# Kernel tuning notes

Hardware: AMD Instinct MI355X
Metric: run time of the kernel (lower is better)

## Reference

```python
import jax, jax.numpy as jnp
import numpy as np


def _gcn_layer(x, W, b, src, dst, norm, n_nodes):
    # PyG GCNConv: h = x @ W, then degree-normalized scatter-add over edges (incl. self loops), then + bias
    h = x @ W                                   # [N, F_out]
    msg = h[src] * norm[:, None]                # [E+N, F_out]
    out = jax.ops.segment_sum(msg, dst, num_segments=n_nodes)
    return out + b


def _norm_and_loops(edge_index, n_nodes):
    # add self loops, compute symmetric normalization deg^-1/2[src]*deg^-1/2[dst]
    loop = jnp.arange(n_nodes, dtype=edge_index.dtype)
    src = jnp.concatenate([edge_index[0], loop])
    dst = jnp.concatenate([edge_index[1], loop])
    deg = jax.ops.segment_sum(jnp.ones_like(dst, dtype=jnp.float32), dst, num_segments=n_nodes)
    dinv = jnp.where(deg > 0, jax.lax.rsqrt(deg), 0.0)
    norm = dinv[src] * dinv[dst]
    return src, dst, norm


def setup_inputs() -> dict:
    key = jax.random.key(0)
    k1, k2, k3, k4 = jax.random.split(key, 4)
    N, E, F = 100000, 1600000, 512
    x = jax.random.normal(k1, (N, F), dtype=jnp.float32)
    edge_index = jax.random.randint(k2, (2, E), 0, N, dtype=jnp.int64)
    W1 = jax.random.normal(k3, (F, 128), dtype=jnp.float32) * (1.0 / np.sqrt(F))
    b1 = jnp.zeros((128,), dtype=jnp.float32)
    W2 = jax.random.normal(k4, (128, 64), dtype=jnp.float32) * (1.0 / np.sqrt(128))
    b2 = jnp.zeros((64,), dtype=jnp.float32)
    return {"x": x, "edge_index": edge_index, "W1": W1, "b1": b1, "W2": W2, "b2": b2}


def reference(x, edge_index, W1, b1, W2, b2):
    n_nodes = x.shape[0]
    src, dst, norm = _norm_and_loops(edge_index, n_nodes)
    h = jax.nn.relu(_gcn_layer(x, W1, b1, src, dst, norm, n_nodes))
    z = jax.nn.relu(_gcn_layer(h, W2, b2, src, dst, norm, n_nodes))
    return z
```

## Files before the change

kernel.cpp:

```cpp
#include <hip/hip_runtime.h>

#define SCAN_B 1024

using f16x8 = __attribute__((ext_vector_type(8))) _Float16;
using f32x4 = __attribute__((ext_vector_type(4))) float;
typedef _Float16 half4v __attribute__((ext_vector_type(4)));
typedef _Float16 half8v __attribute__((ext_vector_type(8)));


__global__ void zero2_kernel(int* __restrict__ a, int* __restrict__ b, int n) {
  int i = blockIdx.x * blockDim.x + threadIdx.x;
  if (i < n) { a[i] = 0; b[i] = 0; }
}

__global__ void count_kernel(const int* __restrict__ ei, int* __restrict__ cnt, int E) {
  int i = blockIdx.x * blockDim.x + threadIdx.x;
  if (i < E) atomicAdd(&cnt[ei[E + i]], 1);
}

__global__ void scan1_kernel(const int* __restrict__ cnt, int* __restrict__ rowstart,
                             int* __restrict__ bsum, float* __restrict__ dinv, int n) {
  __shared__ int sm[SCAN_B];
  const int t = threadIdx.x;
  const int i = blockIdx.x * SCAN_B + t;
  int c = (i < n) ? cnt[i] : 0;
  if (i < n) dinv[i] = rsqrtf((float)(c + 1));
  int v = (i < n) ? (c + 1) : 0;
  sm[t] = v;
  __syncthreads();
  for (int off = 1; off < SCAN_B; off <<= 1) {
    int x = (t >= off) ? sm[t - off] : 0;
    __syncthreads();
    if (t >= off) sm[t] += x;
    __syncthreads();
  }
  if (i < n) rowstart[i] = sm[t] - v;
  if (t == SCAN_B - 1) bsum[blockIdx.x] = sm[t];
}

__global__ void scan2_kernel(int* __restrict__ bsum, int nb) {
  __shared__ int sm[SCAN_B];
  const int t = threadIdx.x;
  int v = (t < nb) ? bsum[t] : 0;
  sm[t] = v;
  __syncthreads();
  for (int off = 1; off < SCAN_B; off <<= 1) {
    int x = (t >= off) ? sm[t - off] : 0;
    __syncthreads();
    if (t >= off) sm[t] += x;
    __syncthreads();
  }
  if (t < nb) bsum[t] = sm[t] - v;
}

__global__ void scan3_kernel(int* __restrict__ rowstart, const int* __restrict__ bsum, int n) {
  int i = blockIdx.x * blockDim.x + threadIdx.x;
  if (i < n) rowstart[i] += bsum[i / SCAN_B];
}

__global__ void fillself_kernel(const int* __restrict__ ei, int* __restrict__ fillc,
                                const int* __restrict__ rowstart, const int* __restrict__ cnt,
                                const float* __restrict__ dinv, float2* __restrict__ ew,
                                int E, int N) {
  int i = blockIdx.x * blockDim.x + threadIdx.x;
  if (i < E) {
    int s = ei[i];
    int d = ei[E + i];
    int p = atomicAdd(&fillc[d], 1);
    ew[rowstart[d] + p] = make_float2(__int_as_float(s), dinv[s] * dinv[d]);
  } else if (i < E + N) {
    int n = i - E;
    float dn = dinv[n];
    ew[rowstart[n] + cnt[n]] = make_float2(__int_as_float(n), dn * dn);
  }
}

__global__ void wconv2_kernel(const float* __restrict__ W1, _Float16* __restrict__ W1t, int K1, int N1,
                              const float* __restrict__ W2, _Float16* __restrict__ W2t, int K2, int N2) {
  int i = blockIdx.x * blockDim.x + threadIdx.x;
  const int n1 = K1 * N1;
  if (i < n1) {
    int k = i / N1, n = i % N1;
    W1t[(size_t)n * K1 + k] = (_Float16)W1[i];
  } else if (i < n1 + K2 * N2) {
    int j = i - n1;
    int k = j / N2, n = j % N2;
    W2t[(size_t)n * K2 + k] = (_Float16)W2[j];
  }
}


template <int BM, int BN, typename CT>
__global__ void __launch_bounds__(512, 2)
gemm_mfma_kernel(const float* __restrict__ A, const _Float16* __restrict__ Wt,
                 CT* __restrict__ C, int M, int K) {
  constexpr int BK   = 32;
  constexpr int LDK  = 40;
  constexpr int MR   = BM / 2 / 16;
  constexpr int NR   = BN / 4 / 16;
  constexpr int N    = BN;
  constexpr int LDC  = NR * 16 + 4;
  constexpr int SMA  = (BM + BN) * LDK * 2;
  constexpr int SME  = 8 * 16 * LDC * 4;
  constexpr int SMEM = SMA > SME ? SMA : SME;

  __shared__ __align__(16) char smem[SMEM];
  _Float16* Asm = (_Float16*)smem;
  _Float16* Bsm = Asm + (size_t)BM * LDK;

  const int tid  = threadIdx.x;
  const int lane = tid & 63;
  const int w    = tid >> 6;
  const int wm   = w >> 2;
  const int wn   = w & 3;
  const int fr   = lane & 15;
  const int fq   = lane >> 4;
  const int m0   = blockIdx.x * BM;

  const int a_c = tid & 7;
  const int a_m = tid >> 3;
  const int br  = tid >> 2;
  const int bj  = tid & 3;

  float4 av[2];
  uint4  bt;

  auto loadA = [&](int kt) {
#pragma unroll
    for (int p = 0; p < 2; ++p) {
      const int gm = m0 + a_m + 64 * p;
      av[p] = (gm < M) ? *(const float4*)&A[(size_t)gm * K + kt + 4 * a_c]
                       : make_float4(0.f, 0.f, 0.f, 0.f);
    }
  };
  auto loadB = [&](int kt) {
    if (tid < BN * 4) bt = *(const uint4*)&Wt[(size_t)br * K + kt + 8 * bj];
  };

  f32x4 acc[MR][NR] = {};

  loadA(0);
  loadB(0);

  for (int kt = 0; kt < K; kt += BK) {
    __syncthreads();

#pragma unroll
    for (int p = 0; p < 2; ++p) {
      const int r = a_m + 64 * p;
      half4v hv = {(_Float16)av[p].x, (_Float16)av[p].y, (_Float16)av[p].z, (_Float16)av[p].w};
      *(half4v*)((char*)Asm + r * (LDK * 2) + a_c * 8) = hv;
    }
    if (tid < BN * 4) *(uint4*)((char*)Bsm + br * (LDK * 2) + 16 * bj) = bt;
    __syncthreads();

    if (kt + BK < K) {
      loadA(kt + BK);
      loadB(kt + BK);
    }

    f16x8 bfrag[NR];
#pragma unroll
    for (int ni = 0; ni < NR; ++ni) {
      const int r = wn * (NR * 16) + ni * 16 + fr;
      bfrag[ni] = *(const f16x8*)((const char*)Bsm + r * (LDK * 2) + fq * 16);
    }
#pragma unroll
    for (int mi = 0; mi < MR; ++mi) {
      const int r = wm * 64 + mi * 16 + fr;
      f16x8 afrag = *(const f16x8*)((const char*)Asm + r * (LDK * 2) + fq * 16);
#pragma unroll
      for (int ni = 0; ni < NR; ++ni)
        acc[mi][ni] = __builtin_amdgcn_mfma_f32_16x16x32_f16(afrag, bfrag[ni], acc[mi][ni], 0, 0, 0);
    }
  }

  __syncthreads();
  {
    float* cst = (float*)smem + (size_t)w * (16 * LDC);
    constexpr int CPR   = NR * 4;
    constexpr int EPASS = (16 * CPR + 63) / 64;
#pragma unroll
    for (int mi = 0; mi < MR; ++mi) {
#pragma unroll
      for (int ni = 0; ni < NR; ++ni)
#pragma unroll
        for (int r = 0; r < 4; ++r)
          cst[(fq * 4 + r) * LDC + ni * 16 + fr] = acc[mi][ni][r];
#pragma unroll
      for (int p = 0; p < EPASS; ++p) {
        const int idx = p * 64 + lane;
        if (idx < 16 * CPR) {
          const int row = idx / CPR;
          const int ch  = idx % CPR;
          const int gm  = m0 + wm * 64 + mi * 16 + row;
          float4 v = *(const float4*)&cst[row * LDC + ch * 4];
          if (gm < M) {
            if constexpr (sizeof(CT) == 2) {
              half4v hv = {(_Float16)v.x, (_Float16)v.y, (_Float16)v.z, (_Float16)v.w};
              *(half4v*)&C[(size_t)gm * N + wn * (NR * 16) + ch * 4] = hv;
            } else {
              *(float4*)&C[(size_t)gm * N + wn * (NR * 16) + ch * 4] = v;
            }
          }
        }
      }
    }
  }
}


template <int F>
__global__ void agg_kernel(const _Float16* __restrict__ hin, const int* __restrict__ rowstart,
                           const int* __restrict__ cnt, const float2* __restrict__ ew,
                           const float* __restrict__ bias, float* __restrict__ outp, int N) {
  constexpr int LPE = F / 8;
  constexpr int EPW = 64 / LPE;
  const int wave = (int)((blockIdx.x * (size_t)blockDim.x + threadIdx.x) >> 6);
  if (wave >= N) return;
  const int lane = threadIdx.x & 63;
  const int sub  = lane / LPE;
  const int c    = lane % LPE;
  const int n    = wave;

  const int beg = rowstart[n];
  const int end = beg + cnt[n] + 1;

  float acc[8] = {};
  int j = beg + sub;
  for (; j + 3 * EPW < end; j += 4 * EPW) {
    const float2 e0 = ew[j];
    const float2 e1 = ew[j + EPW];
    const float2 e2 = ew[j + 2 * EPW];
    const float2 e3 = ew[j + 3 * EPW];
    const half8v v0 = *(const half8v*)&hin[(size_t)__float_as_int(e0.x) * F + c * 8];
    const half8v v1 = *(const half8v*)&hin[(size_t)__float_as_int(e1.x) * F + c * 8];
    const half8v v2 = *(const half8v*)&hin[(size_t)__float_as_int(e2.x) * F + c * 8];
    const half8v v3 = *(const half8v*)&hin[(size_t)__float_as_int(e3.x) * F + c * 8];
#pragma unroll
    for (int i = 0; i < 8; ++i) {
      acc[i] = fmaf((float)v0[i], e0.y, acc[i]);
      acc[i] = fmaf((float)v1[i], e1.y, acc[i]);
      acc[i] = fmaf((float)v2[i], e2.y, acc[i]);
      acc[i] = fmaf((float)v3[i], e3.y, acc[i]);
    }
  }
  for (; j < end; j += EPW) {
    const float2 e = ew[j];
    const half8v v = *(const half8v*)&hin[(size_t)__float_as_int(e.x) * F + c * 8];
#pragma unroll
    for (int i = 0; i < 8; ++i) acc[i] = fmaf((float)v[i], e.y, acc[i]);
  }

#pragma unroll
  for (int d = LPE; d < 64; d <<= 1)
#pragma unroll
    for (int i = 0; i < 8; ++i) acc[i] += __shfl_xor(acc[i], d);

  if (lane < LPE) {
    const float4 b0 = *(const float4*)&bias[c * 8];
    const float4 b1 = *(const float4*)&bias[c * 8 + 4];
    float4 r0, r1;
    r0.x = fmaxf(acc[0] + b0.x, 0.f);
    r0.y = fmaxf(acc[1] + b0.y, 0.f);
    r0.z = fmaxf(acc[2] + b0.z, 0.f);
    r0.w = fmaxf(acc[3] + b0.w, 0.f);
    r1.x = fmaxf(acc[4] + b1.x, 0.f);
    r1.y = fmaxf(acc[5] + b1.y, 0.f);
    r1.z = fmaxf(acc[6] + b1.z, 0.f);
    r1.w = fmaxf(acc[7] + b1.w, 0.f);
    *(float4*)&outp[(size_t)n * F + c * 8] = r0;
    *(float4*)&outp[(size_t)n * F + c * 8 + 4] = r1;
  }
}


extern "C" void kernel_launch(void* const* d_in, const int* in_sizes, int n_in,
                              void* d_out, int out_size, void* d_ws, size_t ws_size,
                              hipStream_t stream) {
  const float* x  = (const float*)d_in[0];
  const int*   ei = (const int*)d_in[1];
  const float* W1 = (const float*)d_in[2];
  const float* b1 = (const float*)d_in[3];
  const float* W2 = (const float*)d_in[4];
  const float* b2 = (const float*)d_in[5];
  float* out = (float*)d_out;

  const int F1 = in_sizes[3];
  const int F2 = in_sizes[5];
  const int F0 = in_sizes[2] / F1;
  const int N  = in_sizes[0] / F0;
  const int E  = in_sizes[1] / 2;

  char* ws = (char*)d_ws;
  size_t off = 0;
  auto alloc = [&](size_t bytes) -> void* {
    void* p = ws + off;
    off = (off + bytes + 255) & ~(size_t)255;
    return p;
  };

  int*    cnt      = (int*)alloc((size_t)N * 4);
  int*    fillc    = (int*)alloc((size_t)N * 4);
  int*    rowstart = (int*)alloc((size_t)N * 4);
  float*  dinv     = (float*)alloc((size_t)N * 4);
  const int nb     = (N + SCAN_B - 1) / SCAN_B;
  int*    bsum     = (int*)alloc((size_t)nb * 4);
  float2* ew       = (float2*)alloc(((size_t)E + N) * 8);
  _Float16* h      = (_Float16*)alloc((size_t)N * F1 * 2);
  float*  h1       = (float*)alloc((size_t)N * F1 * 4);
  _Float16* h2     = h;
  _Float16* W1t    = (_Float16*)alloc((size_t)F0 * F1 * 2);
  _Float16* W2t    = (_Float16*)alloc((size_t)F1 * F2 * 2);

  zero2_kernel<<<(N + 255) / 256, 256, 0, stream>>>(cnt, fillc, N);
  count_kernel<<<(E + 255) / 256, 256, 0, stream>>>(ei, cnt, E);
  scan1_kernel<<<nb, SCAN_B, 0, stream>>>(cnt, rowstart, bsum, dinv, N);
  scan2_kernel<<<1, SCAN_B, 0, stream>>>(bsum, nb);
  scan3_kernel<<<(N + 255) / 256, 256, 0, stream>>>(rowstart, bsum, N);
  fillself_kernel<<<(E + N + 255) / 256, 256, 0, stream>>>(ei, fillc, rowstart, cnt, dinv, ew, E, N);
  wconv2_kernel<<<(F0 * F1 + F1 * F2 + 255) / 256, 256, 0, stream>>>(
      W1, W1t, F0, F1, W2, W2t, F1, F2);

  gemm_mfma_kernel<128, 128, _Float16><<<(N + 127) / 128, 512, 0, stream>>>(x, W1t, h, N, F0);
  {
    const long blocks = ((long)N * 64 + 255) / 256;
    agg_kernel<128><<<(int)blocks, 256, 0, stream>>>(h, rowstart, cnt, ew, b1, h1, N);
  }

  gemm_mfma_kernel<128, 64, _Float16><<<(N + 127) / 128, 512, 0, stream>>>(h1, W2t, h2, N, F1);
  {
    const long blocks = ((long)N * 64 + 255) / 256;
    agg_kernel<64><<<(int)blocks, 256, 0, stream>>>(h2, rowstart, cnt, ew, b2, out, N);
  }
}
```

Measured before the change: 358.4 us.

## Load GEMM MFMA fragments directly from global memory, dropping LDS staging

The GEMM kernel no longer stages A and W tiles through shared memory with double-buffered register prefetch and per-tile barriers. Each lane now reads its MFMA fragments straight from global memory (A as two float4 converted to fp16, W as one f16x8), and the k-loop is unrolled by 4. This removes the LDS traffic and the two syncthreads per k-step. In exchange, A rows are read redundantly by the four wn warps and accesses are less coalesced, so the kernel relies on cache hits. A wave barrier is added before each epilogue patch write.

```diff
diff --git a/kernel.cpp b/kernel.cpp
--- a/kernel.cpp
+++ b/kernel.cpp
@@ -94,19 +94,12 @@
 __global__ void __launch_bounds__(512, 2)
 gemm_mfma_kernel(const float* __restrict__ A, const _Float16* __restrict__ Wt,
                  CT* __restrict__ C, int M, int K) {
-  constexpr int BK   = 32;
-  constexpr int LDK  = 40;
-  constexpr int MR   = BM / 2 / 16;
-  constexpr int NR   = BN / 4 / 16;
-  constexpr int N    = BN;
-  constexpr int LDC  = NR * 16 + 4;
-  constexpr int SMA  = (BM + BN) * LDK * 2;
-  constexpr int SME  = 8 * 16 * LDC * 4;
-  constexpr int SMEM = SMA > SME ? SMA : SME;
-
-  __shared__ __align__(16) char smem[SMEM];
-  _Float16* Asm = (_Float16*)smem;
-  _Float16* Bsm = Asm + (size_t)BM * LDK;
+  constexpr int MR  = BM / 2 / 16;
+  constexpr int NR  = BN / 4 / 16;
+  constexpr int N   = BN;
+  constexpr int LDC = NR * 16 + 4;
+
+  __shared__ __align__(16) float cpatch[8 * 16 * LDC];
 
   const int tid  = threadIdx.x;
   const int lane = tid & 63;
@@ -117,71 +110,45 @@
   const int fq   = lane >> 4;
   const int m0   = blockIdx.x * BM;
 
-  const int a_c = tid & 7;
-  const int a_m = tid >> 3;
-  const int br  = tid >> 2;
-  const int bj  = tid & 3;
-
-  float4 av[2];
-  uint4  bt;
-
-  auto loadA = [&](int kt) {
-#pragma unroll
-    for (int p = 0; p < 2; ++p) {
-      const int gm = m0 + a_m + 64 * p;
-      av[p] = (gm < M) ? *(const float4*)&A[(size_t)gm * K + kt + 4 * a_c]
-                       : make_float4(0.f, 0.f, 0.f, 0.f);
-    }
-  };
-  auto loadB = [&](int kt) {
-    if (tid < BN * 4) bt = *(const uint4*)&Wt[(size_t)br * K + kt + 8 * bj];
-  };
+  size_t abase[MR];
+#pragma unroll
+  for (int mi = 0; mi < MR; ++mi) {
+    const int gm = m0 + wm * 64 + mi * 16 + fr;
+    abase[mi] = (size_t)(gm < M ? gm : 0) * K;
+  }
+  size_t bbase[NR];
+#pragma unroll
+  for (int ni = 0; ni < NR; ++ni)
+    bbase[ni] = (size_t)(wn * (NR * 16) + ni * 16 + fr) * K;
 
   f32x4 acc[MR][NR] = {};
 
-  loadA(0);
-  loadB(0);
-
-  for (int kt = 0; kt < K; kt += BK) {
-    __syncthreads();
-
-#pragma unroll
-    for (int p = 0; p < 2; ++p) {
-      const int r = a_m + 64 * p;
-      half4v hv = {(_Float16)av[p].x, (_Float16)av[p].y, (_Float16)av[p].z, (_Float16)av[p].w};
-      *(half4v*)((char*)Asm + r * (LDK * 2) + a_c * 8) = hv;
-    }
-    if (tid < BN * 4) *(uint4*)((char*)Bsm + br * (LDK * 2) + 16 * bj) = bt;
-    __syncthreads();
-
-    if (kt + BK < K) {
-      loadA(kt + BK);
-      loadB(kt + BK);
-    }
-
+#pragma unroll 4
+  for (int kt = 0; kt < K; kt += 32) {
+    const int k0 = kt + fq * 8;
     f16x8 bfrag[NR];
 #pragma unroll
-    for (int ni = 0; ni < NR; ++ni) {
-      const int r = wn * (NR * 16) + ni * 16 + fr;
-      bfrag[ni] = *(const f16x8*)((const char*)Bsm + r * (LDK * 2) + fq * 16);
-    }
+    for (int ni = 0; ni < NR; ++ni)
+      bfrag[ni] = *(const f16x8*)&Wt[bbase[ni] + k0];
 #pragma unroll
     for (int mi = 0; mi < MR; ++mi) {
-      const int r = wm * 64 + mi * 16 + fr;
-      f16x8 afrag = *(const f16x8*)((const char*)Asm + r * (LDK * 2) + fq * 16);
+      const float4 u = *(const float4*)&A[abase[mi] + k0];
+      const float4 v = *(const float4*)&A[abase[mi] + k0 + 4];
+      f16x8 afrag = {(_Float16)u.x, (_Float16)u.y, (_Float16)u.z, (_Float16)u.w,
+                     (_Float16)v.x, (_Float16)v.y, (_Float16)v.z, (_Float16)v.w};
 #pragma unroll
       for (int ni = 0; ni < NR; ++ni)
         acc[mi][ni] = __builtin_amdgcn_mfma_f32_16x16x32_f16(afrag, bfrag[ni], acc[mi][ni], 0, 0, 0);
     }
   }
 
-  __syncthreads();
   {
-    float* cst = (float*)smem + (size_t)w * (16 * LDC);
+    float* cst = cpatch + (size_t)w * (16 * LDC);
     constexpr int CPR   = NR * 4;
     constexpr int EPASS = (16 * CPR + 63) / 64;
 #pragma unroll
     for (int mi = 0; mi < MR; ++mi) {
+      __builtin_amdgcn_s_barrier();
 #pragma unroll
       for (int ni = 0; ni < NR; ++ni)
 #pragma unroll
```

Result: slower. 492.1 us (+37.3%).
